# Kernel optimization log

Hardware: AMD Instinct MI355X
Metric: run time of the kernel (lower is better)

The kernel has to match this reference:

```python
import jax, jax.numpy as jnp
import numpy as np

NEG = -1e9  # finite stand-in for -inf so downstream grads stay finite
NUM_HEADS = 16


def phm_linear(x, A, S, b):
    # PHM weight: W = sum_i kron(A[i], S[i]) -> (n*kin, n*kout)
    n, kin, kout = S.shape
    W = jnp.einsum('nab,nkl->akbl', A, S).reshape(n * kin, n * kout)
    return x @ W + b


def layer_norm(x, g, b, eps=1e-5):
    mu = jnp.mean(x, axis=-1, keepdims=True)
    var = jnp.var(x, axis=-1, keepdims=True)
    return (x - mu) / jnp.sqrt(var + eps) * g + b


def masking(V, lens):
    # DAG transition mask: vertex i may transition to j>i with j < len[b].
    i = jnp.arange(V)
    tri = i[None, :] > i[:, None]                       # (V,V) j > i
    valid = i[None, None, :] < lens[:, None, None]      # (B,1,V)
    m = tri[None, :, :] & valid
    dead = ~m.any(-1)                                   # (B,V) rows with no valid successor
    eye = jnp.eye(V, dtype=bool)
    m = m | (dead[:, :, None] & eye[None])              # keep softmax finite on dead rows
    return m, dead


def setup_inputs() -> dict:
    key = jax.random.key(0)
    ks = jax.random.split(key, 8)
    B, V, E, VOC = 8, 512, 1024, 32000
    s = 0.02
    return {
        'x': jax.random.normal(ks[0], (B, V, E), jnp.float32),
        'vertex_lens': jax.random.randint(ks[1], (B,), V // 2, V + 1),
        'ln_g': jnp.ones((E,), jnp.float32),
        'ln_b': jnp.zeros((E,), jnp.float32),
        'attn_A': jax.random.normal(ks[2], (4, 4, 4), jnp.float32) * 0.5,
        'attn_S': jax.random.normal(ks[3], (4, 256, 512), jnp.float32) * s,
        'attn_b': jnp.zeros((2 * E,), jnp.float32),
        'gate_A': jax.random.normal(ks[4], (4, 4, 4), jnp.float32) * 0.5,
        'gate_S': jax.random.normal(ks[5], (4, 256, 4), jnp.float32) * s,
        'gate_b': jnp.zeros((NUM_HEADS,), jnp.float32),
        'lm_A': jax.random.normal(ks[6], (2, 2, 2), jnp.float32) * 0.5,
        'lm_S': jax.random.normal(ks[7], (2, 512, 16000), jnp.float32) * s,
        'lm_b': jnp.zeros((VOC,), jnp.float32),
    }


def reference(x, vertex_lens, ln_g, ln_b, attn_A, attn_S, attn_b,
              gate_A, gate_S, gate_b, lm_A, lm_S, lm_b):
    B, V, E = x.shape
    H = NUM_HEADS
    cs = E // H
    xn = layer_norm(x, ln_g, ln_b)
    m, r = masking(V, vertex_lens)
    # gate over heads (B,V,H)
    g = jax.nn.log_softmax(phm_linear(xn, gate_A, gate_S, gate_b), axis=-1)
    qk = phm_linear(xn, attn_A, attn_S, attn_b)
    q, k = jnp.split(qk, 2, axis=-1)
    q = q.reshape(B, V, H, cs)
    k = k.reshape(B, V, H, cs)
    scores = jnp.einsum('bihf,bjhf->bijh', q, k) / jnp.asarray(np.sqrt(cs), jnp.float32)
    scores = jnp.where(m[..., None], scores, NEG)
    scores = jax.nn.log_softmax(scores, axis=2)          # normalize over successors j
    scores = jnp.where(r[:, :, None, None], NEG, scores)  # kill rows past length
    transition_matrix = jax.nn.logsumexp(scores + g[:, :, None, :], axis=-1)  # (B,V,V)
    vocab_log_probs = jax.nn.log_softmax(phm_linear(xn, lm_A, lm_S, lm_b), axis=-1)
    return transition_matrix, vocab_log_probs
```

## Files before the change

kernel.cpp:

```cpp
#include <hip/hip_runtime.h>
#include <hip/hip_bf16.h>
#include <hip/hip_fp8.h>
#include <stdint.h>

typedef __bf16 bf16x8 __attribute__((ext_vector_type(8)));
typedef __bf16 bf16x4 __attribute__((ext_vector_type(4)));
typedef float  f32x4  __attribute__((ext_vector_type(4)));
typedef int    i32x4  __attribute__((ext_vector_type(4)));
typedef int    i32x8  __attribute__((ext_vector_type(8)));

typedef __attribute__((address_space(3))) unsigned int as3_uint;
typedef const __attribute__((address_space(1))) unsigned int as1_uint;

#define NEGC (-1e9f)

__device__ __forceinline__ void async16(void* ldsPtr, const void* gPtr) {
    __builtin_amdgcn_global_load_lds((as1_uint*)(uintptr_t)gPtr,
                                     (as3_uint*)(uintptr_t)ldsPtr, 16, 0, 0);
}

__global__ __launch_bounds__(256) void ln_kernel(const float* __restrict__ x,
                                                 const float* __restrict__ gw,
                                                 const float* __restrict__ bw,
                                                 __bf16* __restrict__ xn,
                                                 unsigned char* __restrict__ xn8) {
    __shared__ float red[8];
    size_t row = blockIdx.x;
    int t = threadIdx.x;
    const float4* xr = (const float4*)(x + row * 1024);
    float4 v = xr[t];
    float s  = v.x + v.y + v.z + v.w;
    float ss = v.x*v.x + v.y*v.y + v.z*v.z + v.w*v.w;
    #pragma unroll
    for (int o = 32; o; o >>= 1) { s += __shfl_xor(s, o); ss += __shfl_xor(ss, o); }
    int wave = t >> 6, lane = t & 63;
    if (lane == 0) { red[wave*2] = s; red[wave*2+1] = ss; }
    __syncthreads();
    float S  = red[0] + red[2] + red[4] + red[6];
    float SS = red[1] + red[3] + red[5] + red[7];
    float mu  = S * (1.0f/1024.0f);
    float var = SS * (1.0f/1024.0f) - mu*mu;
    float rs  = rsqrtf(var + 1e-5f);
    float4 gv = ((const float4*)gw)[t];
    float4 bv = ((const float4*)bw)[t];
    float f0 = (v.x-mu)*rs*gv.x + bv.x;
    float f1 = (v.y-mu)*rs*gv.y + bv.y;
    float f2 = (v.z-mu)*rs*gv.z + bv.z;
    float f3 = (v.w-mu)*rs*gv.w + bv.w;
    bf16x4 o4;
    o4[0] = (__bf16)f0; o4[1] = (__bf16)f1; o4[2] = (__bf16)f2; o4[3] = (__bf16)f3;
    ((bf16x4*)(xn + row*1024))[t] = o4;
    unsigned int pk = (unsigned)__hip_fp8_e4m3(f0).__x
                    | ((unsigned)__hip_fp8_e4m3(f1).__x << 8)
                    | ((unsigned)__hip_fp8_e4m3(f2).__x << 16)
                    | ((unsigned)__hip_fp8_e4m3(f3).__x << 24);
    ((unsigned int*)(xn8 + row*1024))[t] = pk;
}

template<int OUT>
__global__ __launch_bounds__(256) void phm_build(const float* __restrict__ A,
                                                 const float* __restrict__ S,
                                                 void* __restrict__ Wt,
                                                 int nn, int kin, int kout) {
    __shared__ float sh[4][32][65];
    __shared__ float shA[64];
    int t  = threadIdx.x;
    int l0 = blockIdx.x * 64;
    int k0 = blockIdx.y * 32;
    int kt = nn * kin;
    if (t < nn*nn*nn) shA[t] = A[t];
    for (int n = 0; n < nn; ++n) {
        #pragma unroll
        for (int i = 0; i < 8; ++i) {
            int e = t + i*256;
            int kk = e >> 6, ll = e & 63;
            sh[n][kk][ll] = S[((size_t)(n*kin) + k0 + kk)*kout + l0 + ll];
        }
    }
    __syncthreads();
    for (int a = 0; a < nn; ++a)
        for (int b = 0; b < nn; ++b) {
            #pragma unroll
            for (int i = 0; i < 8; ++i) {
                int e = t + i*256;
                int kk = e & 31, ll = e >> 5;
                float val = 0.f;
                for (int n = 0; n < nn; ++n)
                    val += shA[(n*nn + a)*nn + b] * sh[n][kk][ll];
                size_t idx = (size_t)(b*kout + l0 + ll)*kt + a*kin + k0 + kk;
                if (OUT == 0) ((__bf16*)Wt)[idx] = (__bf16)val;
                else          ((unsigned char*)Wt)[idx] = __hip_fp8_e4m3(val * 16.0f).__x;
            }
        }
}

__global__ __launch_bounds__(256) void gatew_kernel(const float* __restrict__ A,
                                                    const float* __restrict__ S,
                                                    float* __restrict__ W) {
    int idx = blockIdx.x*256 + threadIdx.x;
    int r = idx >> 4, c = idx & 15;
    int a = r >> 8, k = r & 255, b = c >> 2, l = c & 3;
    float v = 0.f;
    #pragma unroll
    for (int n = 0; n < 4; ++n)
        v += A[(n*4 + a)*4 + b] * S[((size_t)(n*256 + k))*4 + l];
    W[idx] = v;
}

template<int SWZ, int OUTMODE>
__global__ __launch_bounds__(256) void gemm_mx(const unsigned char* __restrict__ A8,
                                               const unsigned char* __restrict__ B8,
                                               const float* __restrict__ bias,
                                               void* __restrict__ Cv,
                                               int N, int K) {
    __shared__ __align__(16) unsigned char As[128*128];
    __shared__ __align__(16) unsigned char Bs[128*128];
    int tid = threadIdx.x;
    int wave = tid >> 6, lane = tid & 63;
    int m0, n0;
    if (SWZ) {
        int bid  = blockIdx.x;
        int wg   = (bid & 7) * 1000 + (bid >> 3);
        int band = wg / 2000;
        int rem  = wg % 2000;
        m0 = (band * 8 + (rem & 7)) * 128;
        n0 = (rem >> 3) * 128;
    } else {
        m0 = blockIdx.y * 128; n0 = blockIdx.x * 128;
    }
    int wm = (wave >> 1) * 64, wn = (wave & 1) * 64;
    int lrow = lane & 15, lk = lane >> 4;
    f32x4 acc[4][4] = {};
    for (int k0 = 0; k0 < K; k0 += 128) {
        #pragma unroll
        for (int q = 0; q < 4; ++q) {
            int o = q*4096 + tid*16;
            int r = o >> 7;
            int p = (o >> 4) & 7;
            int g = p ^ (r & 7);
            async16((char*)As + q*4096 + wave*1024,
                    (const char*)A8 + (size_t)(m0+r)*K + k0 + g*16);
            async16((char*)Bs + q*4096 + wave*1024,
                    (const char*)B8 + (size_t)(n0+r)*K + k0 + g*16);
        }
        __syncthreads();
        i32x8 af[4], bfr[4];
        #pragma unroll
        for (int mi = 0; mi < 4; ++mi) {
            int r = wm + mi*16 + lrow;
            int c0 = lk*2;
            i32x4 lo = *(const i32x4*)(As + r*128 + ((c0    ^ (r&7))*16));
            i32x4 hi = *(const i32x4*)(As + r*128 + (((c0+1) ^ (r&7))*16));
            af[mi] = __builtin_shufflevector(lo, hi, 0,1,2,3,4,5,6,7);
        }
        #pragma unroll
        for (int ni = 0; ni < 4; ++ni) {
            int r = wn + ni*16 + lrow;
            int c0 = lk*2;
            i32x4 lo = *(const i32x4*)(Bs + r*128 + ((c0    ^ (r&7))*16));
            i32x4 hi = *(const i32x4*)(Bs + r*128 + (((c0+1) ^ (r&7))*16));
            bfr[ni] = __builtin_shufflevector(lo, hi, 0,1,2,3,4,5,6,7);
        }
        #pragma unroll
        for (int mi = 0; mi < 4; ++mi)
            #pragma unroll
            for (int ni = 0; ni < 4; ++ni)
                acc[mi][ni] = __builtin_amdgcn_mfma_scale_f32_16x16x128_f8f6f4(
                    af[mi], bfr[ni], acc[mi][ni],
                    0 , 0 , 0, 127, 0, 127);
        __syncthreads();
    }
    #pragma unroll
    for (int ni = 0; ni < 4; ++ni) {
        int col = n0 + wn + ni*16 + lrow;
        float bv = bias ? bias[col] : 0.f;
        #pragma unroll
        for (int mi = 0; mi < 4; ++mi) {
            #pragma unroll
            for (int r = 0; r < 4; ++r) {
                int rowg = m0 + wm + mi*16 + lk*4 + r;
                float val = acc[mi][ni][r] * 0.0625f + bv;
                if (OUTMODE == 1)
                    ((__bf16*)((char*)Cv + (size_t)rowg * N * 4))[col] = (__bf16)val;
                else
                    ((float*)Cv)[(size_t)rowg * N + col] = val;
            }
        }
    }
}

__global__ __launch_bounds__(256) void gate_kernel(const __bf16* __restrict__ xn,
                                                   const float* __restrict__ Wg,
                                                   const float* __restrict__ gb,
                                                   float* __restrict__ Gp) {
    __shared__ float xr[16][65];
    __shared__ float red[16][17];
    size_t row = blockIdx.x;
    int t = threadIdx.x;
    bf16x4 v = ((const bf16x4*)(xn + row*1024))[t];
    #pragma unroll
    for (int q = 0; q < 4; ++q) {
        int e = t*4 + q;
        xr[e >> 6][e & 63] = (float)v[q];
    }
    __syncthreads();
    int h = t & 15, sl = t >> 4;
    float p = 0.f;
    #pragma unroll
    for (int u = 0; u < 64; ++u) p += xr[sl][u] * Wg[(sl*64 + u)*16 + h];
    red[sl][h] = p;
    __syncthreads();
    if (t < 16) {
        float logit = gb[t];
        #pragma unroll
        for (int s2 = 0; s2 < 16; ++s2) logit += red[s2][t];
        float m = logit;
        #pragma unroll
        for (int o = 8; o; o >>= 1) m = fmaxf(m, __shfl_xor(m, o, 16));
        float e = __expf(logit - m);
        float ssum = e;
        #pragma unroll
        for (int o = 8; o; o >>= 1) ssum += __shfl_xor(ssum, o, 16);
        Gp[row*16 + t] = e / ssum;
    }
}

__global__ __launch_bounds__(512) void scores_kernel(const float* __restrict__ qk,
                                                     const float* __restrict__ Gp,
                                                     const int* __restrict__ lens,
                                                     float* __restrict__ out) {
    __shared__ __align__(16) float qsh[2][16][64];
    __shared__ float gps[16][16];
    __shared__ float wredB[2][8][16];
    int bid = blockIdx.x;
    int b   = bid & 7;
    int i0  = (bid >> 3) * 16;
    int t   = threadIdx.x;
    int wave = t >> 6, lane = t & 63;
    int len = lens[b];
    if (t < 256) {
        int ti = t >> 4;
        gps[ti][t & 15] = Gp[((size_t)b*512 + i0 + ti)*16 + (t & 15)];
        int u = t & 15;
        ((float4*)qsh[0][ti])[u] =
            *(const float4*)(qk + ((size_t)b*512 + i0 + ti)*2048 + u*4);
    }
    int j = t;
    const float4* kp = (const float4*)(qk + ((size_t)b*512 + j)*2048 + 1024);
    bool wlive = ((wave*64 + 63) > i0) && (wave*64 < len);
    float acc[16] = {}, mace[16] = {};
    __syncthreads();
    for (int h = 0; h < 16; ++h) {
        int cur = h & 1;
        if (h + 1 < 16 && t < 256) {
            int ti = t >> 4, u = t & 15;
            ((float4*)qsh[cur^1][ti])[u] =
                *(const float4*)(qk + ((size_t)b*512 + i0 + ti)*2048 + (h+1)*64 + u*4);
        }
        float pex[16];
        if (wlive) {
            float4 kv[16];
            #pragma unroll
            for (int u = 0; u < 16; ++u) kv[u] = kp[h*16 + u];
            #pragma unroll
            for (int ti = 0; ti < 16; ++ti) {
                const float* qrow = qsh[cur][ti];
                float d = 0.f;
                #pragma unroll
                for (int u = 0; u < 16; ++u)
                    d += kv[u].x*qrow[u*4+0] + kv[u].y*qrow[u*4+1]
                       + kv[u].z*qrow[u*4+2] + kv[u].w*qrow[u*4+3];
                int i = i0 + ti;
                float sc = (j > i && j < len) ? d * 0.125f : NEGC;
                float pe = __expf(sc);
                pex[ti] = pe;
                float vv = pe;
                #pragma unroll
                for (int o = 32; o; o >>= 1) vv += __shfl_xor(vv, o);
                if (lane == 0) wredB[cur][wave][ti] = vv;
            }
        } else {
            #pragma unroll
            for (int ti = 0; ti < 16; ++ti) pex[ti] = 0.f;
            if (lane == 0) {
                #pragma unroll
                for (int ti = 0; ti < 16; ++ti) wredB[cur][wave][ti] = 0.f;
            }
        }
        __syncthreads();
        #pragma unroll
        for (int ti = 0; ti < 16; ++ti) {
            float gs = 0.f;
            #pragma unroll
            for (int w = 0; w < 8; ++w) gs += wredB[cur][w][ti];
            float inv = 1.0f / gs;
            float g = gps[ti][h];
            acc[ti]  += pex[ti] * inv * g;
            mace[ti] += g * inv;
        }
    }
    #pragma unroll
    for (int ti = 0; ti < 16; ++ti) {
        int i = i0 + ti;
        float val;
        if (i >= len - 1)            val = NEGC;
        else if (j > i && j < len)   val = __logf(acc[ti]);
        else                         val = NEGC + __logf(mace[ti]);
        out[((size_t)b*512 + i)*512 + j] = val;
    }
}

__global__ __launch_bounds__(256) void vocab_softmax_bf16(float* __restrict__ out) {
    __shared__ float red[8];
    size_t row = blockIdx.x;
    char* rowbase = (char*)out + row * (size_t)32000 * 4;
    const bf16x8* g8 = (const bf16x8*)rowbase;
    int t = threadIdx.x, wave = t >> 6, lane = t & 63;
    bf16x8 cc[16];
    float mx = -1e30f;
    #pragma unroll
    for (int s = 0; s < 16; ++s) {
        int v = t + s*256;
        if (v < 4000) {
            cc[s] = g8[v];
            #pragma unroll
            for (int jj = 0; jj < 8; ++jj) mx = fmaxf(mx, (float)cc[s][jj]);
        }
    }
    #pragma unroll
    for (int o = 32; o; o >>= 1) mx = fmaxf(mx, __shfl_xor(mx, o));
    if (lane == 0) red[wave] = mx;
    __syncthreads();
    mx = fmaxf(fmaxf(red[0], red[1]), fmaxf(red[2], red[3]));
    float sum = 0.f;
    #pragma unroll
    for (int s = 0; s < 16; ++s) {
        int v = t + s*256;
        if (v < 4000) {
            #pragma unroll
            for (int jj = 0; jj < 8; ++jj) sum += __expf((float)cc[s][jj] - mx);
        }
    }
    #pragma unroll
    for (int o = 32; o; o >>= 1) sum += __shfl_xor(sum, o);
    if (lane == 0) red[4 + wave] = sum;
    __syncthreads();
    float lse = mx + __logf(red[4] + red[5] + red[6] + red[7]);
    float4* o4 = (float4*)rowbase;
    #pragma unroll
    for (int s = 0; s < 16; ++s) {
        int v = t + s*256;
        if (v < 4000) {
            float4 a, b;
            a.x = (float)cc[s][0] - lse; a.y = (float)cc[s][1] - lse;
            a.z = (float)cc[s][2] - lse; a.w = (float)cc[s][3] - lse;
            b.x = (float)cc[s][4] - lse; b.y = (float)cc[s][5] - lse;
            b.z = (float)cc[s][6] - lse; b.w = (float)cc[s][7] - lse;
            o4[v*2]   = a;
            o4[v*2+1] = b;
        }
    }
}

extern "C" void kernel_launch(void* const* d_in, const int* in_sizes, int n_in,
                              void* d_out, int out_size, void* d_ws, size_t ws_size,
                              hipStream_t stream) {
    (void)in_sizes; (void)n_in; (void)out_size; (void)ws_size;
    const float* x      = (const float*)d_in[0];
    const int*   lens   = (const int*)  d_in[1];
    const float* ln_g   = (const float*)d_in[2];
    const float* ln_b   = (const float*)d_in[3];
    const float* attn_A = (const float*)d_in[4];
    const float* attn_S = (const float*)d_in[5];
    const float* attn_b = (const float*)d_in[6];
    const float* gate_A = (const float*)d_in[7];
    const float* gate_S = (const float*)d_in[8];
    const float* gate_b = (const float*)d_in[9];
    const float* lm_A   = (const float*)d_in[10];
    const float* lm_S   = (const float*)d_in[11];
    const float* lm_b   = (const float*)d_in[12];

    float* out_trans = (float*)d_out;
    float* out_vocab = out_trans + (size_t)8*512*512;

    char* ws = (char*)d_ws;
    __bf16*        xn      = (__bf16*)(ws);
    unsigned char* xn8     = (unsigned char*)(ws + 8388608);
    unsigned char* WtAttn8 = (unsigned char*)(ws + 12582912);
    unsigned char* WtLm8   = (unsigned char*)(ws + 14680064);
    float*         Wg      = (float*)(ws + 47448064);
    float*         qkbuf   = (float*)(ws + 47513600);
    float*         Gp      = (float*)(ws + 81068032);

    hipLaunchKernelGGL(ln_kernel,    dim3(4096),     dim3(256), 0, stream, x, ln_g, ln_b, xn, xn8);
    hipLaunchKernelGGL(gatew_kernel, dim3(64),       dim3(256), 0, stream, gate_A, gate_S, Wg);
    hipLaunchKernelGGL((phm_build<1>), dim3(8, 8),   dim3(256), 0, stream, attn_A, attn_S, (void*)WtAttn8, 4, 256, 512);
    hipLaunchKernelGGL((phm_build<1>), dim3(250, 16),dim3(256), 0, stream, lm_A, lm_S, (void*)WtLm8, 2, 512, 16000);
    hipLaunchKernelGGL((gemm_mx<0,0>), dim3(16, 32), dim3(256), 0, stream,
                       xn8, WtAttn8, attn_b, (void*)qkbuf, 2048, 1024);
    hipLaunchKernelGGL(gate_kernel,  dim3(4096),     dim3(256), 0, stream, xn, Wg, gate_b, Gp);
    hipLaunchKernelGGL(scores_kernel,dim3(256),      dim3(512), 0, stream, qkbuf, Gp, lens, out_trans);
    hipLaunchKernelGGL((gemm_mx<1,1>), dim3(8000),   dim3(256), 0, stream,
                       xn8, WtLm8, lm_b, (void*)out_vocab, 32000, 1024);
    hipLaunchKernelGGL(vocab_softmax_bf16, dim3(4096), dim3(256), 0, stream, out_vocab);
}
```

Before: 714.4 us.

## Restructure scores kernel: 8 rows per block, two columns per thread

The scores kernel now uses 256-thread blocks, each covering 8 query rows instead of 16. Each thread handles two successor columns, and the block preloads all 8 full query rows into LDS once instead of double-buffering per head. The dead-wave skip is removed, so every thread always loads k and computes dot products. The aim is to double the block count to 512 for better CU coverage and to drop the per-head q staging. In exchange, the k vectors are reloaded twice as often across blocks, register pressure rises from holding two k slices, and masked regions are no longer skipped.

```diff
diff --git a/kernel.cpp b/kernel.cpp
--- a/kernel.cpp
+++ b/kernel.cpp
@@ -225,88 +225,81 @@
     }
 }
 
-__global__ __launch_bounds__(512) void scores_kernel(const float* __restrict__ qk,
+__global__ __launch_bounds__(256) void scores_kernel(const float* __restrict__ qk,
                                                      const float* __restrict__ Gp,
                                                      const int* __restrict__ lens,
                                                      float* __restrict__ out) {
-    __shared__ __align__(16) float qsh[2][16][64];
-    __shared__ float gps[16][16];
-    __shared__ float wredB[2][8][16];
+    __shared__ float qs[8][1024];
+    __shared__ float gps[8][16];
+    __shared__ float wredB[2][4][8];
     int bid = blockIdx.x;
     int b   = bid & 7;
-    int i0  = (bid >> 3) * 16;
+    int i0  = (bid >> 3) * 8;
     int t   = threadIdx.x;
     int wave = t >> 6, lane = t & 63;
     int len = lens[b];
-    if (t < 256) {
-        int ti = t >> 4;
-        gps[ti][t & 15] = Gp[((size_t)b*512 + i0 + ti)*16 + (t & 15)];
-        int u = t & 15;
-        ((float4*)qsh[0][ti])[u] =
-            *(const float4*)(qk + ((size_t)b*512 + i0 + ti)*2048 + u*4);
-    }
-    int j = t;
-    const float4* kp = (const float4*)(qk + ((size_t)b*512 + j)*2048 + 1024);
-    bool wlive = ((wave*64 + 63) > i0) && (wave*64 < len);
-    float acc[16] = {}, mace[16] = {};
-    __syncthreads();
+    const float4* qbase = (const float4*)(qk + ((size_t)b*512 + i0)*2048);
+    #pragma unroll
+    for (int s = 0; s < 8; ++s) {
+        int e = t + s*256;
+        int ti = e >> 8, c4 = e & 255;
+        ((float4*)qs)[e] = qbase[ti*512 + c4];
+    }
+    if (t < 128) gps[t >> 4][t & 15] = Gp[((size_t)b*512 + i0 + (t >> 4))*16 + (t & 15)];
+    __syncthreads();
+    int j0 = t, j1 = t + 256;
+    const float4* kp0 = (const float4*)(qk + ((size_t)b*512 + j0)*2048 + 1024);
+    const float4* kp1 = (const float4*)(qk + ((size_t)b*512 + j1)*2048 + 1024);
+    float acc0[8] = {}, acc1[8] = {}, mace[8] = {};
     for (int h = 0; h < 16; ++h) {
-        int cur = h & 1;
-        if (h + 1 < 16 && t < 256) {
-            int ti = t >> 4, u = t & 15;
-            ((float4*)qsh[cur^1][ti])[u] =
-                *(const float4*)(qk + ((size_t)b*512 + i0 + ti)*2048 + (h+1)*64 + u*4);
-        }
-        float pex[16];
-        if (wlive) {
-            float4 kv[16];
-            #pragma unroll
-            for (int u = 0; u < 16; ++u) kv[u] = kp[h*16 + u];
-            #pragma unroll
-            for (int ti = 0; ti < 16; ++ti) {
-                const float* qrow = qsh[cur][ti];
-                float d = 0.f;
-                #pragma unroll
-                for (int u = 0; u < 16; ++u)
-                    d += kv[u].x*qrow[u*4+0] + kv[u].y*qrow[u*4+1]
-                       + kv[u].z*qrow[u*4+2] + kv[u].w*qrow[u*4+3];
-                int i = i0 + ti;
-                float sc = (j > i && j < len) ? d * 0.125f : NEGC;
-                float pe = __expf(sc);
-                pex[ti] = pe;
-                float vv = pe;
-                #pragma unroll
-                for (int o = 32; o; o >>= 1) vv += __shfl_xor(vv, o);
-                if (lane == 0) wredB[cur][wave][ti] = vv;
+        float4 kv0[16], kv1[16];
+        #pragma unroll
+        for (int u = 0; u < 16; ++u) { kv0[u] = kp0[h*16 + u]; kv1[u] = kp1[h*16 + u]; }
+        float pex0[8], pex1[8];
+        #pragma unroll
+        for (int ti = 0; ti < 8; ++ti) {
+            const float* qrow = &qs[ti][h*64];
+            float d0 = 0.f, d1 = 0.f;
+            #pragma unroll
+            for (int u = 0; u < 16; ++u) {
+                float q0 = qrow[u*4+0], q1 = qrow[u*4+1], q2 = qrow[u*4+2], q3 = qrow[u*4+3];
+                d0 += kv0[u].x*q0 + kv0[u].y*q1 + kv0[u].z*q2 + kv0[u].w*q3;
+                d1 += kv1[u].x*q0 + kv1[u].y*q1 + kv1[u].z*q2 + kv1[u].w*q3;
             }
-        } else {
-            #pragma unroll
-            for (int ti = 0; ti < 16; ++ti) pex[ti] = 0.f;
-            if (lane == 0) {
-                #pragma unroll
-                for (int ti = 0; ti < 16; ++ti) wredB[cur][wave][ti] = 0.f;
-            }
+            int i = i0 + ti;
+            float sc0 = (j0 > i && j0 < len) ? d0 * 0.125f : NEGC;
+            float sc1 = (j1 > i && j1 < len) ? d1 * 0.125f : NEGC;
+            float pe0 = __expf(sc0), pe1 = __expf(sc1);
+            pex0[ti] = pe0; pex1[ti] = pe1;
+            float vv = pe0 + pe1;
+            #pragma unroll
+            for (int o = 32; o; o >>= 1) vv += __shfl_xor(vv, o);
+            if (lane == 0) wredB[h & 1][wave][ti] = vv;
         }
         __syncthreads();
         #pragma unroll
-        for (int ti = 0; ti < 16; ++ti) {
-            float gs = 0.f;
-            #pragma unroll
-            for (int w = 0; w < 8; ++w) gs += wredB[cur][w][ti];
+        for (int ti = 0; ti < 8; ++ti) {
+            float gs = wredB[h & 1][0][ti] + wredB[h & 1][1][ti]
+                     + wredB[h & 1][2][ti] + wredB[h & 1][3][ti];
             float inv = 1.0f / gs;
             float g = gps[ti][h];
-            acc[ti]  += pex[ti] * inv * g;
+            acc0[ti] += pex0[ti] * inv * g;
+            acc1[ti] += pex1[ti] * inv * g;
             mace[ti] += g * inv;
         }
     }
     #pragma unroll
-    for (int ti = 0; ti < 16; ++ti) {
+    for (int ti = 0; ti < 8; ++ti) {
         int i = i0 + ti;
-        float val;
-        if (i >= len - 1)            val = NEGC;
-        else if (j > i && j < len)   val = __logf(acc[ti]);
-        else                         val = NEGC + __logf(mace[ti]);
-        out[((size_t)b*512 + i)*512 + j] = val;
+        float lm = NEGC + __logf(mace[ti]);
+        float v0, v1;
+        if (i >= len - 1) { v0 = NEGC; v1 = NEGC; }
+        else {
+            v0 = (j0 > i && j0 < len) ? __logf(acc0[ti]) : lm;
+            v1 = (j1 > i && j1 < len) ? __logf(acc1[ti]) : lm;
+        }
+        out[((size_t)b*512 + i)*512 + j0] = v0;
+        out[((size_t)b*512 + i)*512 + j1] = v1;
     }
 }
 
@@ -399,7 +392,7 @@
     hipLaunchKernelGGL((gemm_mx<0,0>), dim3(16, 32), dim3(256), 0, stream,
                        xn8, WtAttn8, attn_b, (void*)qkbuf, 2048, 1024);
     hipLaunchKernelGGL(gate_kernel,  dim3(4096),     dim3(256), 0, stream, xn, Wg, gate_b, Gp);
-    hipLaunchKernelGGL(scores_kernel,dim3(256),      dim3(512), 0, stream, qkbuf, Gp, lens, out_trans);
+    hipLaunchKernelGGL(scores_kernel,dim3(512),      dim3(256), 0, stream, qkbuf, Gp, lens, out_trans);
     hipLaunchKernelGGL((gemm_mx<1,1>), dim3(8000),   dim3(256), 0, stream,
                        xn8, WtLm8, lm_b, (void*)out_vocab, 32000, 1024);
     hipLaunchKernelGGL(vocab_softmax_bf16, dim3(4096), dim3(256), 0, stream, out_vocab);
```

New measurement: 673.3 us (median of 2 runs). 1.06x faster.
